# Kernel optimization log

Measured on AMD Instinct MI355X. Metric: run time of the kernel, lower is better.

Reference implementation:

```python
import jax, jax.numpy as jnp
import numpy as np

B, C, L = 16, 512, 8192
K = 7  # kernel_size, symmetric padding K//2 = 3


def setup_inputs() -> dict:
    key = jax.random.key(0)
    k1, k2, k3 = jax.random.split(key, 3)
    x = jax.random.normal(k1, (B, C, L), dtype=jnp.float32)
    mask = jax.random.randint(k2, (B, 1, L), 0, 2).astype(bool)
    # Conv1d(2 -> 1, kernel 7, no bias): weight shape (out=1, in=2, k=7)
    conv_w = jax.random.normal(k3, (1, 2, K), dtype=jnp.float32) * (1.0 / np.sqrt(2 * K))
    return {"x": x, "mask": mask, "conv_w": conv_w}


def reference(x, mask, conv_w):
    # Channel-wise max and mean pooling -> (B, 1, L) each
    max_c = jnp.max(x, axis=1, keepdims=True)
    avg_c = jnp.mean(x, axis=1, keepdims=True)
    # NOTE: in the original torch code, every masked_fill_ call uses the
    # out-of-place masked_fill and its return value is discarded, so the mask
    # has NO effect on the computation. We replicate that faithfully: `mask`
    # is accepted but unused.
    feats = jnp.concatenate([max_c, avg_c], axis=1)  # (B, 2, L)
    logits = jax.lax.conv_general_dilated(
        feats, conv_w,
        window_strides=(1,),
        padding=[(K // 2, K // 2)],
        dimension_numbers=("NCH", "OIH", "NCH"),
    )  # (B, 1, L)
    attn = jax.nn.sigmoid(logits)
    return attn * x  # (B, C, L)
```

## Files before the change

kernel.cpp:

```cpp
#include <hip/hip_runtime.h>
#include <math.h>

#define NB 16
#define NC 512
#define NL 8192
#define KW 7

#define TILE 64
#define HALO (KW / 2)
#define TIN  (TILE - 2 * HALO)
#define NTILES ((NL + TIN - 1) / TIN)
#define CG  16
#define CPT (NC / CG)

__global__ __launch_bounds__(1024) void sam1d_fused(
    const float* __restrict__ x, const float* __restrict__ w,
    float* __restrict__ out) {
    __shared__ float lds_mx[CG * TILE];
    __shared__ float lds_sm[CG * TILE];
    __shared__ float pool_mx[TILE];
    __shared__ float pool_av[TILE];

    const int tid  = threadIdx.x;
    const int lcol = tid & (TILE - 1);
    const int cg   = tid >> 6;
    const int blk  = blockIdx.x;
    const int b    = blk / NTILES;
    const int t    = blk - b * NTILES;
    const int l    = t * TIN - HALO + lcol;
    const bool lvalid = (l >= 0) && (l < NL);

    const float* px = x + (size_t)b * NC * NL + (size_t)(cg * CPT) * NL + l;

    float xv[CPT];
    if (lvalid) {
#pragma unroll
        for (int j = 0; j < CPT; ++j) xv[j] = px[(size_t)j * NL];
    } else {
#pragma unroll
        for (int j = 0; j < CPT; ++j) xv[j] = 0.0f;
    }

    float mx = xv[0], sm = xv[0];
#pragma unroll
    for (int j = 1; j < CPT; ++j) { mx = fmaxf(mx, xv[j]); sm += xv[j]; }

#pragma unroll
    for (int j = 0; j < CPT; ++j) asm volatile("" : "+v"(xv[j]));

    lds_mx[cg * TILE + lcol] = mx;
    lds_sm[cg * TILE + lcol] = sm;
    __syncthreads();

    if (tid < TILE) {
        float m = lds_mx[tid];
#pragma unroll
        for (int g = 1; g < CG; ++g) m = fmaxf(m, lds_mx[g * TILE + tid]);
        const int gl = t * TIN - HALO + tid;
        pool_mx[tid] = (gl >= 0 && gl < NL) ? m : 0.0f;
    } else if (tid < 2 * TILE) {
        const int c = tid - TILE;
        float s = lds_sm[c];
#pragma unroll
        for (int g = 1; g < CG; ++g) s += lds_sm[g * TILE + c];
        const int gl = t * TIN - HALO + c;
        pool_av[c] = (gl >= 0 && gl < NL) ? s * (1.0f / (float)NC) : 0.0f;
    }
    __syncthreads();

    if (lcol >= HALO && lcol < HALO + TIN && l < NL) {
        float logit = 0.0f;
#pragma unroll
        for (int k = 0; k < KW; ++k) {
            logit = fmaf(pool_mx[lcol - HALO + k], w[k],      logit);
            logit = fmaf(pool_av[lcol - HALO + k], w[KW + k], logit);
        }
        const float attn = 1.0f / (1.0f + expf(-logit));
        float* po = out + (size_t)b * NC * NL + (size_t)(cg * CPT) * NL + l;
#pragma unroll
        for (int j = 0; j < CPT; ++j) po[(size_t)j * NL] = attn * xv[j];
    }
}

extern "C" void kernel_launch(void* const* d_in, const int* in_sizes, int n_in,
                              void* d_out, int out_size, void* d_ws, size_t ws_size,
                              hipStream_t stream) {
    const float* x = (const float*)d_in[0];
    const float* w = (const float*)d_in[2];
    float* out = (float*)d_out;

    const int blocks = NB * NTILES;
    sam1d_fused<<<blocks, 1024, 0, stream>>>(x, w, out);
}
```

Before: 164.5 us.

## Vectorize x loads/stores as float4 and regroup threads as 16 columns by 64 channel groups

Each thread now handles four consecutive positions with float4 loads and stores across 8 channels, instead of one position across 32 channels. The tile keeps 64 columns but is aligned to 4 with a 4-column left halo, so each block computes 56 outputs. The aim is wider, fewer memory transactions on this bandwidth-bound kernel. The cost is a 64-deep LDS reduction per column and fewer independent loads in flight per thread. The LDS arrays are padded to avoid bank conflicts.

```diff
diff --git a/kernel.cpp b/kernel.cpp
--- a/kernel.cpp
+++ b/kernel.cpp
@@ -7,78 +7,99 @@
 #define KW 7
 
 #define TILE 64
-#define HALO (KW / 2)
-#define TIN  (TILE - 2 * HALO)
+#define TIN  56
 #define NTILES ((NL + TIN - 1) / TIN)
-#define CG  16
-#define CPT (NC / CG)
+#define NF4  16
+#define CG   64
+#define CPT  8
 
 __global__ __launch_bounds__(1024) void sam1d_fused(
     const float* __restrict__ x, const float* __restrict__ w,
     float* __restrict__ out) {
-    __shared__ float lds_mx[CG * TILE];
-    __shared__ float lds_sm[CG * TILE];
+    __shared__ float lds_mx[CG][TILE + 1];
+    __shared__ float lds_sm[CG][TILE + 1];
     __shared__ float pool_mx[TILE];
     __shared__ float pool_av[TILE];
 
     const int tid  = threadIdx.x;
-    const int lcol = tid & (TILE - 1);
-    const int cg   = tid >> 6;
-    const int blk  = blockIdx.x;
-    const int b    = blk / NTILES;
-    const int t    = blk - b * NTILES;
-    const int l    = t * TIN - HALO + lcol;
-    const bool lvalid = (l >= 0) && (l < NL);
+    const int f4   = tid & (NF4 - 1);
+    const int cg   = tid >> 4;
+    const int b    = blockIdx.x / NTILES;
+    const int t    = blockIdx.x - b * NTILES;
+    const int base = t * TIN;
+    const int c0   = base - 4 + 4 * f4;
+    const bool valid = (c0 >= 0) && (c0 < NL);
 
-    const float* px = x + (size_t)b * NC * NL + (size_t)(cg * CPT) * NL + l;
+    const float* px = x + ((size_t)b * NC + (size_t)cg * CPT) * NL + c0;
 
-    float xv[CPT];
-    if (lvalid) {
+    float4 xv[CPT];
+    if (valid) {
 #pragma unroll
-        for (int j = 0; j < CPT; ++j) xv[j] = px[(size_t)j * NL];
+        for (int j = 0; j < CPT; ++j)
+            xv[j] = *(const float4*)(px + (size_t)j * NL);
     } else {
 #pragma unroll
-        for (int j = 0; j < CPT; ++j) xv[j] = 0.0f;
+        for (int j = 0; j < CPT; ++j) xv[j] = make_float4(0.f, 0.f, 0.f, 0.f);
     }
 
-    float mx = xv[0], sm = xv[0];
+    float4 mx = xv[0], sm = xv[0];
 #pragma unroll
-    for (int j = 1; j < CPT; ++j) { mx = fmaxf(mx, xv[j]); sm += xv[j]; }
+    for (int j = 1; j < CPT; ++j) {
+        mx.x = fmaxf(mx.x, xv[j].x); sm.x += xv[j].x;
+        mx.y = fmaxf(mx.y, xv[j].y); sm.y += xv[j].y;
+        mx.z = fmaxf(mx.z, xv[j].z); sm.z += xv[j].z;
+        mx.w = fmaxf(mx.w, xv[j].w); sm.w += xv[j].w;
+    }
 
 #pragma unroll
-    for (int j = 0; j < CPT; ++j) asm volatile("" : "+v"(xv[j]));
+    for (int j = 0; j < CPT; ++j)
+        asm volatile("" : "+v"(xv[j].x), "+v"(xv[j].y), "+v"(xv[j].z), "+v"(xv[j].w));
 
-    lds_mx[cg * TILE + lcol] = mx;
-    lds_sm[cg * TILE + lcol] = sm;
+    const int lc = 4 * f4;
+    lds_mx[cg][lc + 0] = mx.x;  lds_sm[cg][lc + 0] = sm.x;
+    lds_mx[cg][lc + 1] = mx.y;  lds_sm[cg][lc + 1] = sm.y;
+    lds_mx[cg][lc + 2] = mx.z;  lds_sm[cg][lc + 2] = sm.z;
+    lds_mx[cg][lc + 3] = mx.w;  lds_sm[cg][lc + 3] = sm.w;
     __syncthreads();
 
     if (tid < TILE) {
-        float m = lds_mx[tid];
+        float m = lds_mx[0][tid];
 #pragma unroll
-        for (int g = 1; g < CG; ++g) m = fmaxf(m, lds_mx[g * TILE + tid]);
-        const int gl = t * TIN - HALO + tid;
+        for (int g = 1; g < CG; ++g) m = fmaxf(m, lds_mx[g][tid]);
+        const int gl = base - 4 + tid;
         pool_mx[tid] = (gl >= 0 && gl < NL) ? m : 0.0f;
     } else if (tid < 2 * TILE) {
         const int c = tid - TILE;
-        float s = lds_sm[c];
+        float s = lds_sm[0][c];
 #pragma unroll
-        for (int g = 1; g < CG; ++g) s += lds_sm[g * TILE + c];
-        const int gl = t * TIN - HALO + c;
+        for (int g = 1; g < CG; ++g) s += lds_sm[g][c];
+        const int gl = base - 4 + c;
         pool_av[c] = (gl >= 0 && gl < NL) ? s * (1.0f / (float)NC) : 0.0f;
     }
     __syncthreads();
 
-    if (lcol >= HALO && lcol < HALO + TIN && l < NL) {
-        float logit = 0.0f;
+    if (f4 >= 1 && f4 <= 14 && c0 < NL) {
+        float attn[4];
 #pragma unroll
-        for (int k = 0; k < KW; ++k) {
-            logit = fmaf(pool_mx[lcol - HALO + k], w[k],      logit);
-            logit = fmaf(pool_av[lcol - HALO + k], w[KW + k], logit);
+        for (int q = 0; q < 4; ++q) {
+            float logit = 0.0f;
+#pragma unroll
+            for (int k = 0; k < KW; ++k) {
+                logit = fmaf(pool_mx[lc + q + k - 3], w[k],      logit);
+                logit = fmaf(pool_av[lc + q + k - 3], w[KW + k], logit);
+            }
+            attn[q] = 1.0f / (1.0f + expf(-logit));
         }
-        const float attn = 1.0f / (1.0f + expf(-logit));
-        float* po = out + (size_t)b * NC * NL + (size_t)(cg * CPT) * NL + l;
+        float* po = out + ((size_t)b * NC + (size_t)cg * CPT) * NL + c0;
 #pragma unroll
-        for (int j = 0; j < CPT; ++j) po[(size_t)j * NL] = attn * xv[j];
+        for (int j = 0; j < CPT; ++j) {
+            float4 o;
+            o.x = attn[0] * xv[j].x;
+            o.y = attn[1] * xv[j].y;
+            o.z = attn[2] * xv[j].z;
+            o.w = attn[3] * xv[j].w;
+            *(float4*)(po + (size_t)j * NL) = o;
+        }
     }
 }
 
```

New measurement: 146.1 us. -11.2%, faster.
